# Kernel optimization log

Hardware: AMD Instinct MI355X
Metric: run time of the kernel (lower is better)

Reference implementation:

```python
import jax, jax.numpy as jnp
import numpy as np

IN_FEATURES = 8192
OUT_FEATURES = 512
N_BITS = 8
ABS_RANGE = 4.0
TOP_K = 32
SIZE = IN_FEATURES // N_BITS            # per-bit latent/weight slice size
QUANT_STEP = ABS_RANGE / 2 ** N_BITS
BATCH = 4096


def setup_inputs() -> dict:
    key = jax.random.key(0)
    k1, k2, k3 = jax.random.split(key, 3)
    lim = float(np.sqrt(6.0 / (IN_FEATURES + OUT_FEATURES)))  # xavier_uniform
    latent = jax.random.normal(k1, (BATCH, IN_FEATURES), jnp.float32)
    weight = jax.random.uniform(k2, (IN_FEATURES, OUT_FEATURES), jnp.float32, -lim, lim)
    weight_mirror = jax.random.uniform(k3, (IN_FEATURES, OUT_FEATURES), jnp.float32, -lim, lim)
    return {"latent": latent, "weight": weight, "weight_mirror": weight_mirror}


def _forward(latent, weight, weight_mirror):
    sg = jax.lax.stop_gradient
    B = latent.shape[0]
    # reshape into per-bit slices: latent [B, n_bits, size], weights [n_bits, size, out]
    L = latent.reshape(B, N_BITS, SIZE)
    Wn = weight.reshape(N_BITS, SIZE, OUT_FEATURES)
    Wm = weight_mirror.reshape(N_BITS, SIZE, OUT_FEATURES)
    # sign binarization with straight-through estimator (forward = sign, grad = identity)
    Bsign = sg(jnp.where(Wn >= 0, 1.0, -1.0).astype(Wn.dtype))
    Bsign_m = sg(jnp.where(Wm >= 0, 1.0, -1.0).astype(Wm.dtype))
    Wsum = sg(Bsign + Bsign_m - Wn - Wm) + Wn + Wm  # ste_weight + ste_weight_mirror
    # top-k sparsify each slice, then STE sign of surviving entries
    k = min(TOP_K, SIZE)
    if TOP_K is not None and TOP_K > 0 and k < SIZE:
        _, idx = jax.lax.top_k(L, k)                       # [B, n_bits, k]
        mask = jnp.zeros(L.shape, bool)
        b = jnp.arange(B)[:, None, None]
        n = jnp.arange(N_BITS)[None, :, None]
        mask = mask.at[b, n, idx].set(True)
        Lm = L * mask
        Ls = sg(jnp.sign(Lm) - Lm) + Lm                    # forward = sign(masked), grad = mask
    else:
        Ls = L
    # per-bit scale: 2**(n_bits-i-2) * quant_step
    scales = (2.0 ** (N_BITS - jnp.arange(N_BITS) - 2)).astype(latent.dtype) * jnp.asarray(QUANT_STEP, latent.dtype)
    contrib = jnp.einsum('bns,nso->bno', Ls, Wsum) * scales[None, :, None]  # [B, n_bits, out]
    # reconstruction_i = detach(reconstruction_{i-1}) + contrib_i  ->  detached prefix cumsum
    cum = jnp.cumsum(sg(contrib), axis=1) - sg(contrib) + contrib
    result = jnp.transpose(cum, (1, 0, 2))                 # [n_bits, B, out]
    latent_group = jnp.mean(jnp.sum(jnp.abs(Ls), axis=-1), axis=0)  # [n_bits]
    return latent_group, result


def reference(latent, weight, weight_mirror):
    return _forward(latent, weight, weight_mirror)
```

## Files before the change

### kernel.cpp

```cpp
#include <hip/hip_runtime.h>
#include <stdint.h>

#define NBITS  8
#define SLICE  1024
#define OUTF   512
#define INF    8192
#define TOPK   32
#define BATCHN 4096

#define ROWS    INF
#define DUMMY_B (ROWS * 64 * 4)
#define TBL2_B  ((ROWS + 1) * 64 * 4)

__device__ __forceinline__ uint32_t fkey_u(uint32_t u) {
  uint32_t m = ((uint32_t)((int32_t)u >> 31)) | 0x80000000u;
  return u ^ m;
}
__device__ __forceinline__ float kfloat(uint32_t k) {
  uint32_t u = (k & 0x80000000u) ? (k ^ 0x80000000u) : ~k;
  return __uint_as_float(u);
}

__global__ __launch_bounds__(256) void prep_kernel(
    const float* __restrict__ W, const float* __restrict__ Wm,
    uint32_t* __restrict__ tbl)
{
  int tid = blockIdx.x * blockDim.x + threadIdx.x;
  int r = tid >> 6;
  int w = tid & 63;
  const float* wr = W  + (size_t)r * OUTF;
  const float* mr = Wm + (size_t)r * OUTF;
  uint32_t word = 0;
#pragma unroll
  for (int i = 0; i < 8; ++i) {
    int col = w + 64 * i;
    uint32_t b = (wr[col] >= 0.0f ? 1u : 0u) + (mr[col] >= 0.0f ? 1u : 0u);
    word |= b << (4 * i);
  }
  tbl[tid] = word;
  tbl[(TBL2_B / 4) + tid] = 0x22222222u - word;
  if (tid < 64) tbl[(DUMMY_B / 4) + tid] = 0x11111111u;
}

__global__ __launch_bounds__(512, 4) void main_kernel(
    const float* __restrict__ latent,
    const uint32_t* __restrict__ tbl,
    float* __restrict__ out, int* __restrict__ partial)
{
  __shared__ __align__(16) uint32_t sel[NBITS][TOPK];
  __shared__ float sums[NBITS][OUTF];

  const int b    = blockIdx.x;
  const int wv   = threadIdx.x >> 6;
  const int lane = threadIdx.x & 63;

  const float4* src =
      (const float4*)(latent + (size_t)b * INF + (size_t)wv * SLICE + lane * 16);
  uint32_t key[16];
  uint32_t lmax = 0u;
#pragma unroll
  for (int q = 0; q < 4; ++q) {
    float4 f = src[q];
    float vv[4] = {f.x, f.y, f.z, f.w};
#pragma unroll
    for (int t = 0; t < 4; ++t) {
      uint32_t k = fkey_u(__float_as_uint(vv[t]));
      key[4*q+t] = k;
      lmax = lmax > k ? lmax : k;
    }
  }

  uint32_t bmin = lmax, bmax = lmax;
#pragma unroll
  for (int d = 1; d < 64; d <<= 1) {
    uint32_t tn = (uint32_t)__shfl_xor((int)bmin, d);
    uint32_t tx = (uint32_t)__shfl_xor((int)bmax, d);
    bmin = bmin < tn ? bmin : tn;
    bmax = bmax > tx ? bmax : tx;
  }

  uint32_t T = 0, midE = 0, cE = 0;
  bool fast = false;
  {
    uint32_t lo = bmin, hi = bmax;
    while (lo < hi) {
      uint32_t d   = hi - lo;
      uint32_t mid = lo + (d >> 1) + (d & 1u);
      float fm     = 0.5f * (kfloat(lo) + kfloat(hi));
      uint32_t km  = fkey_u(__float_as_uint(fm));
      if (km > lo && km <= hi) mid = km;
      uint32_t c = 0;
#pragma unroll
      for (int j = 0; j < 16; ++j) c += (key[j] >= mid) ? 1u : 0u;
      int cnt = 0;
#pragma unroll
      for (int bb = 0; bb < 5; ++bb)
        cnt += (int)__popcll(__ballot((c >> bb) & 1u)) << bb;
      if (cnt == TOPK) { fast = true; midE = mid; cE = c; break; }
      if (cnt > TOPK) lo = mid; else hi = mid - 1u;
    }
    if (!fast) T = lo;
  }

  const uint32_t pbase = ((uint32_t)(wv * SLICE + lane * 16)) << 8;
  int nzl = 0;

  if (fast) {
    int sc = (int)cE;
#pragma unroll
    for (int dd = 1; dd < 64; dd <<= 1) {
      int t = __shfl_up(sc, dd);
      if (lane >= dd) sc += t;
    }
    int slot = sc - (int)cE;
#pragma unroll
    for (int j = 0; j < 16; ++j) {
      uint32_t kk = key[j];
      if (kk >= midE) {
        bool ispos = kk > 0x80000000u;
        bool isneg = kk < 0x7FFFFFFFu;
        uint32_t off = ispos ? (pbase + (j << 8))
                     : (isneg ? (pbase + (j << 8) + TBL2_B) : (uint32_t)DUMMY_B);
        sel[wv][slot++] = off;
        nzl += (ispos || isneg) ? 1 : 0;
      }
    }
  } else {
    int cgt = 0, ceq = 0;
#pragma unroll
    for (int j = 0; j < 16; ++j) { cgt += (key[j] > T); ceq += (key[j] == T); }
    int packed = (cgt << 16) | ceq;
    int sc = packed;
#pragma unroll
    for (int dd = 1; dd < 64; dd <<= 1) {
      int t = __shfl_up(sc, dd);
      if (lane >= dd) sc += t;
    }
    int tot     = __shfl(sc, 63);
    int total_g = tot >> 16;
    int nties   = TOPK - total_g;
    int excl    = sc - packed;
    int posg    = excl >> 16;
    int pose    = excl & 0xFFFF;
#pragma unroll
    for (int j = 0; j < 16; ++j) {
      uint32_t kk  = key[j];
      bool isgt    = kk > T;
      bool iseq    = (kk == T);
      bool takeeq  = iseq && (pose < nties);
      bool take    = isgt || takeeq;
      bool ispos   = kk > 0x80000000u;
      bool isneg   = kk < 0x7FFFFFFFu;
      uint32_t off = ispos ? (pbase + (j << 8))
                   : (isneg ? (pbase + (j << 8) + TBL2_B) : (uint32_t)DUMMY_B);
      int slot = isgt ? posg : (total_g + pose);
      if (take) sel[wv][slot] = off;
      posg += isgt ? 1 : 0;
      pose += iseq ? 1 : 0;
      nzl  += (take && (ispos || isneg)) ? 1 : 0;
    }
  }

  {
    int cnz = 0;
#pragma unroll
    for (int bb = 0; bb < 5; ++bb)
      cnz += (int)__popcll(__ballot((nzl >> bb) & 1)) << bb;
    if (lane == 0) partial[wv * BATCHN + b] = cnz;
  }

  uint32_t offr[TOPK];
  {
    const uint4* sp = (const uint4*)sel[wv];
#pragma unroll
    for (int q = 0; q < TOPK / 4; ++q) {
      uint4 e4 = sp[q];
      offr[4*q+0] = e4.x; offr[4*q+1] = e4.y;
      offr[4*q+2] = e4.z; offr[4*q+3] = e4.w;
    }
  }
  const uint32_t lb = (uint32_t)lane << 2;
  const char* tbase = (const char*)tbl;
  uint32_t wrd[TOPK];
#pragma unroll
  for (int j = 0; j < TOPK; ++j)
    wrd[j] = *(const uint32_t*)(tbase + (offr[j] + lb));
  __builtin_amdgcn_sched_barrier(0);

  uint32_t acc0 = 0, acc1 = 0, tmp = 0;
  int inch = 0;
#pragma unroll
  for (int j = 0; j < TOPK; ++j) {
    tmp += wrd[j];
    if (++inch == 7 || j == TOPK - 1) {
      acc0 += tmp & 0x0F0F0F0Fu;
      acc1 += (tmp >> 4) & 0x0F0F0F0Fu;
      tmp = 0; inch = 0;
    }
  }

  const float scale_n = 1.0f / (float)(1 << wv);
#pragma unroll
  for (int i2 = 0; i2 < 4; ++i2) {
    int f0 = (int)((acc0 >> (8 * i2)) & 0xFFu);
    int f1 = (int)((acc1 >> (8 * i2)) & 0xFFu);
    sums[wv][lane + 128 * i2]      = scale_n * (float)(2 * f0 - 64);
    sums[wv][lane + 128 * i2 + 64] = scale_n * (float)(2 * f1 - 64);
  }

  __syncthreads();

  const int col = threadIdx.x;
  float racc = 0.0f;
  float* obase = out + 8 + (size_t)b * OUTF + col;
#pragma unroll
  for (int n2 = 0; n2 < NBITS; ++n2) {
    racc += sums[n2][col];
    obase[(size_t)n2 * BATCHN * OUTF] = racc;
  }
}

__global__ __launch_bounds__(512) void fin_kernel(
    const int* __restrict__ partial, float* __restrict__ out)
{
  const int wv   = threadIdx.x >> 6;
  const int lane = threadIdx.x & 63;
  const int* p = partial + wv * BATCHN;
  int s = 0;
#pragma unroll
  for (int k = 0; k < BATCHN / 64; ++k)
    s += p[lane + 64 * k];
#pragma unroll
  for (int d = 32; d >= 1; d >>= 1)
    s += __shfl_down(s, d);
  if (lane == 0) out[wv] = (float)s * (1.0f / (float)BATCHN);
}

extern "C" void kernel_launch(void* const* d_in, const int* in_sizes, int n_in,
                              void* d_out, int out_size, void* d_ws, size_t ws_size,
                              hipStream_t stream)
{
  const float* latent = (const float*)d_in[0];
  const float* W      = (const float*)d_in[1];
  const float* Wm     = (const float*)d_in[2];
  float* out = (float*)d_out;

  int*      partial = (int*)d_ws;
  uint32_t* tbl     = (uint32_t*)((char*)d_ws + 131072);

  prep_kernel<<<(INF * 64) / 256, 256, 0, stream>>>(W, Wm, tbl);
  main_kernel<<<BATCHN, 512, 0, stream>>>(latent, tbl, out, partial);
  fin_kernel<<<1, 512, 0, stream>>>(partial, out);
}
```

Baseline: 70.99 us.

## Split fused kernel into top-k select and table-gather kernels with compact indices

The fused per-batch kernel is split in two. A select kernel, running 256-thread blocks at higher occupancy, computes each slice's top-32 and writes 16-bit codes (row index plus a sign/zero tag) to global memory. A gather kernel reads those codes, decodes table offsets and accumulates the packed sign words. The bisection's first probe also moves from the midpoint to a 0.42 fraction of the range. The aim is to let the register-heavy selection and the latency-bound gathers each run at better occupancy, at the cost of an extra launch and a global round trip for the selection codes.

```diff
diff --git a/kernel.cpp b/kernel.cpp
--- a/kernel.cpp
+++ b/kernel.cpp
@@ -7,10 +7,12 @@
 #define INF    8192
 #define TOPK   32
 #define BATCHN 4096
+#define NSLICE (BATCHN * NBITS)
 
 #define ROWS    INF
 #define DUMMY_B (ROWS * 64 * 4)
 #define TBL2_B  ((ROWS + 1) * 64 * 4)
+
 
 __device__ __forceinline__ uint32_t fkey_u(uint32_t u) {
   uint32_t m = ((uint32_t)((int32_t)u >> 31)) | 0x80000000u;
@@ -42,20 +44,17 @@
   if (tid < 64) tbl[(DUMMY_B / 4) + tid] = 0x11111111u;
 }
 
-__global__ __launch_bounds__(512, 4) void main_kernel(
+__global__ __launch_bounds__(256, 8) void select_kernel(
     const float* __restrict__ latent,
-    const uint32_t* __restrict__ tbl,
-    float* __restrict__ out, int* __restrict__ partial)
-{
-  __shared__ __align__(16) uint32_t sel[NBITS][TOPK];
-  __shared__ float sums[NBITS][OUTF];
-
-  const int b    = blockIdx.x;
-  const int wv   = threadIdx.x >> 6;
-  const int lane = threadIdx.x & 63;
+    uint16_t* __restrict__ selg, int* __restrict__ partial)
+{
+  const int slice = blockIdx.x * 4 + (threadIdx.x >> 6);
+  const int lane  = threadIdx.x & 63;
+  const int b     = slice >> 3;
+  const int nb    = slice & 7;
 
   const float4* src =
-      (const float4*)(latent + (size_t)b * INF + (size_t)wv * SLICE + lane * 16);
+      (const float4*)(latent + (size_t)b * INF + (size_t)nb * SLICE + lane * 16);
   uint32_t key[16];
   uint32_t lmax = 0u;
 #pragma unroll
@@ -83,11 +82,13 @@
   bool fast = false;
   {
     uint32_t lo = bmin, hi = bmax;
+    float frac = 0.42f;
     while (lo < hi) {
       uint32_t d   = hi - lo;
       uint32_t mid = lo + (d >> 1) + (d & 1u);
-      float fm     = 0.5f * (kfloat(lo) + kfloat(hi));
-      uint32_t km  = fkey_u(__float_as_uint(fm));
+      float fl = kfloat(lo), fh = kfloat(hi);
+      uint32_t km = fkey_u(__float_as_uint(fl + frac * (fh - fl)));
+      frac = 0.5f;
       if (km > lo && km <= hi) mid = km;
       uint32_t c = 0;
 #pragma unroll
@@ -102,7 +103,8 @@
     if (!fast) T = lo;
   }
 
-  const uint32_t pbase = ((uint32_t)(wv * SLICE + lane * 16)) << 8;
+  uint16_t* sb = selg + ((size_t)slice << 5);
+  const uint32_t gbase = (uint32_t)(nb * SLICE + lane * 16);
   int nzl = 0;
 
   if (fast) {
@@ -119,9 +121,9 @@
       if (kk >= midE) {
         bool ispos = kk > 0x80000000u;
         bool isneg = kk < 0x7FFFFFFFu;
-        uint32_t off = ispos ? (pbase + (j << 8))
-                     : (isneg ? (pbase + (j << 8) + TBL2_B) : (uint32_t)DUMMY_B);
-        sel[wv][slot++] = off;
+        uint32_t code = ispos ? (gbase + j)
+                      : (isneg ? ((gbase + j) | 0x4000u) : 0x8000u);
+        sb[slot++] = (uint16_t)code;
         nzl += (ispos || isneg) ? 1 : 0;
       }
     }
@@ -151,10 +153,10 @@
       bool take    = isgt || takeeq;
       bool ispos   = kk > 0x80000000u;
       bool isneg   = kk < 0x7FFFFFFFu;
-      uint32_t off = ispos ? (pbase + (j << 8))
-                   : (isneg ? (pbase + (j << 8) + TBL2_B) : (uint32_t)DUMMY_B);
+      uint32_t code = ispos ? (gbase + j)
+                    : (isneg ? ((gbase + j) | 0x4000u) : 0x8000u);
       int slot = isgt ? posg : (total_g + pose);
-      if (take) sel[wv][slot] = off;
+      if (take) sb[slot] = (uint16_t)code;
       posg += isgt ? 1 : 0;
       pose += iseq ? 1 : 0;
       nzl  += (take && (ispos || isneg)) ? 1 : 0;
@@ -166,33 +168,51 @@
 #pragma unroll
     for (int bb = 0; bb < 5; ++bb)
       cnz += (int)__popcll(__ballot((nzl >> bb) & 1)) << bb;
-    if (lane == 0) partial[wv * BATCHN + b] = cnz;
-  }
-
-  uint32_t offr[TOPK];
-  {
-    const uint4* sp = (const uint4*)sel[wv];
-#pragma unroll
-    for (int q = 0; q < TOPK / 4; ++q) {
-      uint4 e4 = sp[q];
-      offr[4*q+0] = e4.x; offr[4*q+1] = e4.y;
-      offr[4*q+2] = e4.z; offr[4*q+3] = e4.w;
-    }
-  }
+    if (lane == 0) partial[nb * BATCHN + b] = cnz;
+  }
+}
+
+__global__ __launch_bounds__(512, 4) void gather_kernel(
+    const uint16_t* __restrict__ selg,
+    const uint32_t* __restrict__ tbl,
+    float* __restrict__ out)
+{
+  __shared__ float sums[NBITS][OUTF];
+
+  const int b    = blockIdx.x;
+  const int lane = threadIdx.x & 63;
+  const int wv   = __builtin_amdgcn_readfirstlane(threadIdx.x >> 6);
+
+  const uint32_t* sp32 =
+      (const uint32_t*)(selg + (((size_t)b * NBITS + wv) << 5));
+  uint32_t code2[16];
+#pragma unroll
+  for (int q = 0; q < 16; ++q) code2[q] = sp32[q];
+
+  const char* tb = (const char*)tbl;
   const uint32_t lb = (uint32_t)lane << 2;
-  const char* tbase = (const char*)tbl;
-  uint32_t wrd[TOPK];
-#pragma unroll
-  for (int j = 0; j < TOPK; ++j)
-    wrd[j] = *(const uint32_t*)(tbase + (offr[j] + lb));
+  uint32_t wrd[32];
+#pragma unroll
+  for (int q = 0; q < 16; ++q) {
+    uint32_t c2 = code2[q];
+#pragma unroll
+    for (int h = 0; h < 2; ++h) {
+      uint32_t e  = (h ? (c2 >> 16) : c2) & 0xFFFFu;
+      uint32_t r  = e & 0x3FFFu;
+      uint32_t t2 = e >> 14;
+      uint32_t byteoff = r * 256u +
+          (t2 == 1u ? (uint32_t)TBL2_B : (t2 == 2u ? (uint32_t)DUMMY_B : 0u));
+      wrd[2*q+h] = *(const uint32_t*)(tb + (size_t)byteoff + lb);
+    }
+  }
   __builtin_amdgcn_sched_barrier(0);
 
   uint32_t acc0 = 0, acc1 = 0, tmp = 0;
   int inch = 0;
 #pragma unroll
-  for (int j = 0; j < TOPK; ++j) {
+  for (int j = 0; j < 32; ++j) {
     tmp += wrd[j];
-    if (++inch == 7 || j == TOPK - 1) {
+    if (++inch == 7 || j == 31) {
       acc0 += tmp & 0x0F0F0F0Fu;
       acc1 += (tmp >> 4) & 0x0F0F0F0Fu;
       tmp = 0; inch = 0;
@@ -246,9 +266,11 @@
   float* out = (float*)d_out;
 
   int*      partial = (int*)d_ws;
-  uint32_t* tbl     = (uint32_t*)((char*)d_ws + 131072);
+  uint16_t* selg    = (uint16_t*)((char*)d_ws + 131072);
+  uint32_t* tbl     = (uint32_t*)((char*)d_ws + 2228224);
 
   prep_kernel<<<(INF * 64) / 256, 256, 0, stream>>>(W, Wm, tbl);
-  main_kernel<<<BATCHN, 512, 0, stream>>>(latent, tbl, out, partial);
+  select_kernel<<<NSLICE / 4, 256, 0, stream>>>(latent, selg, partial);
+  gather_kernel<<<BATCHN, 512, 0, stream>>>(selg, tbl, out);
   fin_kernel<<<1, 512, 0, stream>>>(partial, out);
 }
```

New measurement: 81.19 us. 1.14x slower.
